# Performance work log

Measured on AMD Instinct MI355X. Metric: run time of the kernel, lower is better.

The kernel has to match this reference:

```python
import jax, jax.numpy as jnp
import numpy as np

B, N, D = 2, 1024, 1024
H, DH = 16, 64          # nhead, head_dim (D = H*DH)
FF = 4096               # dim_feedforward = 4*D
E = 8                   # num experts
EPS = 1e-5


def layer_norm(x, s, b):
    m = jnp.mean(x, -1, keepdims=True)
    v = jnp.mean((x - m) ** 2, -1, keepdims=True)
    return (x - m) * jax.lax.rsqrt(v + EPS) * s + b


def moe_gate(x, Wg):
    # top-1 gating: expert index + gate probability per token
    probs = jax.nn.softmax(x @ Wg, axis=-1)            # [B,N,E]
    idx = jnp.argmax(probs, axis=-1)                   # [B,N]
    gw = jnp.take_along_axis(probs, idx[..., None], -1)[..., 0]  # [B,N]
    return idx, gw


def moe_linear(x, W, b, idx, gw):
    # x:[B,N,Din], W:[E,Din,Dout], b:[E,Dout]; route each token to expert idx
    y = jnp.einsum('bnd,edh->bneh', x, W) + b          # [B,N,E,Dout]
    oh = jax.nn.one_hot(idx, E, dtype=x.dtype)         # [B,N,E]
    return jnp.einsum('bneh,bne->bnh', y, oh) * gw[..., None]


def setup_inputs() -> dict:
    key = jax.random.key(0)
    ks = jax.random.split(key, 8)
    g = lambda k, shape, sc: jax.random.normal(k, shape, jnp.float32) * sc
    inv_d = 1.0 / np.sqrt(D)
    return dict(
        src=g(ks[0], (B, N, D), 1.0),
        key_padding_mask=jnp.zeros((B, N), dtype=bool),
        Wg_attn=g(ks[1], (D, E), inv_d),
        Wqkv=g(ks[2], (E, D, 3 * D), inv_d), bqkv=jnp.zeros((E, 3 * D), jnp.float32),
        Wo=g(ks[3], (E, D, D), inv_d), bo=jnp.zeros((E, D), jnp.float32),
        Wg_ffn=g(ks[4], (D, E), inv_d),
        W1=g(ks[5], (E, D, FF), inv_d), b1=jnp.zeros((E, FF), jnp.float32),
        W2=g(ks[6], (E, FF, D), 1.0 / np.sqrt(FF)), b2=jnp.zeros((E, D), jnp.float32),
        ln1_s=jnp.ones((D,), jnp.float32), ln1_b=jnp.zeros((D,), jnp.float32),
        ln2_s=jnp.ones((D,), jnp.float32), ln2_b=jnp.zeros((D,), jnp.float32),
    )


def reference(src, key_padding_mask, Wg_attn, Wqkv, bqkv, Wo, bo,
              Wg_ffn, W1, b1, W2, b2, ln1_s, ln1_b, ln2_s, ln2_b):
    # attention mask: key_padding_mask.unsqueeze(1).unsqueeze(1) * -10000
    mask = jnp.where(key_padding_mask[:, None, None, :], -10000.0, 0.0).astype(src.dtype)

    # --- MoE self-attention (gate decided once, reused for qkv and dense) ---
    idx, gw = moe_gate(src, Wg_attn)
    qkv = moe_linear(src, Wqkv, bqkv, idx, gw)                 # [B,N,3D]
    q, k, v = jnp.split(qkv, 3, axis=-1)
    heads = lambda t: t.reshape(B, N, H, DH).transpose(0, 2, 1, 3)  # [B,H,N,DH]
    q, k, v = heads(q), heads(k), heads(v)
    scores = jnp.einsum('bhqd,bhkd->bhqk', q, k) / np.sqrt(DH) + mask
    probs = jax.nn.softmax(scores, axis=-1)
    ctx = jnp.einsum('bhqk,bhkd->bhqd', probs, v)
    ctx = ctx.transpose(0, 2, 1, 3).reshape(B, N, D)
    attn_out = moe_linear(ctx, Wo, bo, idx, gw)

    # post-norm residual
    x = layer_norm(src + attn_out, ln1_s, ln1_b)

    # --- MoE FFN (its own gate, shared across both linears) ---
    fidx, fgw = moe_gate(x, Wg_ffn)
    h = jax.nn.gelu(moe_linear(x, W1, b1, fidx, fgw))
    ffn = moe_linear(h, W2, b2, fidx, fgw)

    return layer_norm(x + ffn, ln2_s, ln2_b)
```

## Files before the change

### kernel.cpp

```cpp
#include <hip/hip_runtime.h>


#define B_   2
#define N_   1024
#define D_   1024
#define H_   16
#define DH_  64
#define FF_  4096
#define E_   8
#define NTOK 2048

typedef __attribute__((ext_vector_type(8))) short short8;
typedef __attribute__((ext_vector_type(8))) unsigned short ushort8;
typedef __attribute__((ext_vector_type(4))) unsigned short ushort4v;
typedef __attribute__((ext_vector_type(4))) float f32x4;

__device__ inline unsigned short f2bf(float f) {
  unsigned u = __float_as_uint(f);
  u += 0x7FFFu + ((u >> 16) & 1u);
  return (unsigned short)(u >> 16);
}

__device__ inline float gelu_tanh(float x) {
  float x3 = x * x * x;
  float t = tanhf(0.7978845608028654f * (x + 0.044715f * x3));
  return 0.5f * x * (1.0f + t);
}

__global__ __launch_bounds__(256) void gate_kernel(
    const float* __restrict__ X, const float* __restrict__ Wg,
    int* __restrict__ idx, float* __restrict__ gwv, int* __restrict__ cnt) {
  int t = blockIdx.x * 4 + (threadIdx.x >> 6);
  int lane = threadIdx.x & 63;
  const float* x = X + (size_t)t * D_;
  float acc[E_];
#pragma unroll
  for (int j = 0; j < E_; j++) acc[j] = 0.f;
#pragma unroll
  for (int i = 0; i < 16; i++) {
    int d = i * 64 + lane;
    float xv = x[d];
    const float4* w = (const float4*)(Wg + (size_t)d * E_);
    float4 w0 = w[0], w1 = w[1];
    acc[0] += xv * w0.x; acc[1] += xv * w0.y; acc[2] += xv * w0.z; acc[3] += xv * w0.w;
    acc[4] += xv * w1.x; acc[5] += xv * w1.y; acc[6] += xv * w1.z; acc[7] += xv * w1.w;
  }
#pragma unroll
  for (int o = 1; o < 64; o <<= 1) {
#pragma unroll
    for (int j = 0; j < E_; j++) acc[j] += __shfl_xor(acc[j], o, 64);
  }
  float m = acc[0]; int bi = 0;
#pragma unroll
  for (int j = 1; j < E_; j++) { if (acc[j] > m) { m = acc[j]; bi = j; } }
  float den = 0.f;
#pragma unroll
  for (int j = 0; j < E_; j++) den += expf(acc[j] - m);
  float gw = expf(acc[bi] - m) / den;
  if (lane == 0) { idx[t] = bi; gwv[t] = gw; atomicAdd(&cnt[bi], 1); }
}

__global__ __launch_bounds__(256) void route_kernel(
    const int* __restrict__ idx, const int* __restrict__ cnt,
    int* __restrict__ off, int* __restrict__ perm, int ntok) {
  __shared__ int loff[E_ + 1];
  __shared__ int lfill[E_];
  if (threadIdx.x == 0) {
    int s = 0;
    for (int e = 0; e < E_; e++) { loff[e] = s; s += cnt[e]; }
    loff[E_] = s;
  }
  if (threadIdx.x < E_) lfill[threadIdx.x] = 0;
  __syncthreads();
  for (int t = (int)threadIdx.x; t < ntok; t += 256) {
    int e = idx[t];
    int p = atomicAdd(&lfill[e], 1);
    perm[loff[e] + p] = t;
  }
  if (threadIdx.x < E_ + 1) off[threadIdx.x] = loff[threadIdx.x];
}

__global__ __launch_bounds__(256) void transpose_w_kernel(
    const float* __restrict__ W, unsigned short* __restrict__ WT, int K, int N) {
  __shared__ float T[64][68];
  int e = blockIdx.z;
  int n0 = blockIdx.x * 64, k0 = blockIdx.y * 64;
  int tid = threadIdx.x;
  {
    int kr = tid >> 4;
    int nc = (tid & 15) * 4;
#pragma unroll
    for (int j = 0; j < 4; j++) {
      int k = kr + j * 16;
      float4 v = *(const float4*)(W + ((size_t)e * K + k0 + k) * N + n0 + nc);
      *(float4*)&T[k][nc] = v;
    }
  }
  __syncthreads();
  {
    int n = tid & 63;
    int ko = (tid >> 6) * 16;
    ushort8 o0, o1;
#pragma unroll
    for (int i = 0; i < 8; i++) o0[i] = f2bf(T[ko + i][n]);
#pragma unroll
    for (int i = 0; i < 8; i++) o1[i] = f2bf(T[ko + 8 + i][n]);
    unsigned short* p = WT + ((size_t)e * N + n0 + n) * K + k0 + ko;
    *(ushort8*)p = o0;
    *(ushort8*)(p + 8) = o1;
  }
}

template <typename AT, int KS>
__global__ __launch_bounds__(256) void gemm_kernel(
    const AT* __restrict__ A, int ldA,
    const unsigned short* __restrict__ WT,
    const int* __restrict__ perm, const int* __restrict__ off,
    float* __restrict__ part, int K, int N) {
  __shared__ __align__(16) unsigned short As[128][40];
  __shared__ __align__(16) unsigned short Bs[128][40];
  __shared__ int toks[128];

  int e = blockIdx.y;
  int base = off[e];
  int cnt = off[e + 1] - base;
  int mt = blockIdx.z / KS;
  int kc = blockIdx.z % KS;
  int m0 = mt * 128;
  if (m0 >= cnt) return;
  int rows_valid = min(128, cnt - m0);
  int tid = threadIdx.x;
  if (tid < 128) {
    int r = (tid < rows_valid) ? tid : (rows_valid - 1);
    toks[tid] = perm[base + m0 + r];
  }
  int nb = blockIdx.x * 128;
  int lane = tid & 63, wave = tid >> 6;
  int wm = (wave >> 1) * 64, wn = (wave & 1) * 64;
  int lr = lane & 15, lg = lane >> 4;
  f32x4 acc[4][4];
#pragma unroll
  for (int m = 0; m < 4; m++)
#pragma unroll
    for (int n = 0; n < 4; n++) acc[m][n] = (f32x4){0.f, 0.f, 0.f, 0.f};
  int srow = tid >> 1, koff = (tid & 1) * 16;
  int KL = K / KS;
  int kbeg = kc * KL;
  __syncthreads();

  for (int k0 = kbeg; k0 < kbeg + KL; k0 += 32) {
    {
      const AT* ar = A + (size_t)toks[srow] * ldA + k0 + koff;
      ushort8 o0, o1;
      if constexpr (sizeof(AT) == 4) {
        const float* fa = (const float*)ar;
        float4 v0 = *(const float4*)(fa);
        float4 v1 = *(const float4*)(fa + 4);
        float4 v2 = *(const float4*)(fa + 8);
        float4 v3 = *(const float4*)(fa + 12);
        o0[0] = f2bf(v0.x); o0[1] = f2bf(v0.y); o0[2] = f2bf(v0.z); o0[3] = f2bf(v0.w);
        o0[4] = f2bf(v1.x); o0[5] = f2bf(v1.y); o0[6] = f2bf(v1.z); o0[7] = f2bf(v1.w);
        o1[0] = f2bf(v2.x); o1[1] = f2bf(v2.y); o1[2] = f2bf(v2.z); o1[3] = f2bf(v2.w);
        o1[4] = f2bf(v3.x); o1[5] = f2bf(v3.y); o1[6] = f2bf(v3.z); o1[7] = f2bf(v3.w);
      } else {
        o0 = *(const ushort8*)ar;
        o1 = *(const ushort8*)(ar + 8);
      }
      *(ushort8*)&As[srow][koff] = o0;
      *(ushort8*)&As[srow][koff + 8] = o1;
      const unsigned short* br = WT + ((size_t)e * N + nb + srow) * K + k0 + koff;
      *(ushort8*)&Bs[srow][koff] = *(const ushort8*)br;
      *(ushort8*)&Bs[srow][koff + 8] = *(const ushort8*)(br + 8);
    }
    __syncthreads();
    short8 av[4], bv[4];
#pragma unroll
    for (int m = 0; m < 4; m++) av[m] = *(const short8*)&As[wm + m * 16 + lr][lg * 8];
#pragma unroll
    for (int n = 0; n < 4; n++) bv[n] = *(const short8*)&Bs[wn + n * 16 + lr][lg * 8];
#pragma unroll
    for (int m = 0; m < 4; m++)
#pragma unroll
      for (int n = 0; n < 4; n++)
        acc[m][n] = __builtin_amdgcn_mfma_f32_16x16x32_bf16(av[m], bv[n], acc[m][n], 0, 0, 0);
    __syncthreads();
  }

  float* pr = part + (size_t)kc * ((size_t)NTOK * N);
#pragma unroll
  for (int n = 0; n < 4; n++) {
    int col = nb + wn + n * 16 + lr;
#pragma unroll
    for (int m = 0; m < 4; m++) {
#pragma unroll
      for (int reg = 0; reg < 4; reg++) {
        int r = wm + m * 16 + lg * 4 + reg;
        if (r < rows_valid)
          pr[(size_t)toks[r] * N + col] = acc[m][n][reg];
      }
    }
  }
}

template <int KS, bool GELU, bool OBF16>
__global__ __launch_bounds__(256) void reduce_kernel(
    const float* __restrict__ part, const float* __restrict__ bias,
    const float* __restrict__ gwv, const int* __restrict__ idx,
    void* __restrict__ out, int N) {
  int t = blockIdx.y;
  int n = (blockIdx.x * 256 + threadIdx.x) * 4;
  int e = idx[t];
  float gw = gwv[t];
  const float* p = part + (size_t)t * N + n;
  float4 a = *(const float4*)p;
#pragma unroll
  for (int k = 1; k < KS; k++) {
    float4 q = *(const float4*)(p + (size_t)k * NTOK * N);
    a.x += q.x; a.y += q.y; a.z += q.z; a.w += q.w;
  }
  float4 bv = *(const float4*)(bias + (size_t)e * N + n);
  a.x = (a.x + bv.x) * gw; a.y = (a.y + bv.y) * gw;
  a.z = (a.z + bv.z) * gw; a.w = (a.w + bv.w) * gw;
  if constexpr (GELU) {
    a.x = gelu_tanh(a.x); a.y = gelu_tanh(a.y);
    a.z = gelu_tanh(a.z); a.w = gelu_tanh(a.w);
  }
  if constexpr (OBF16) {
    ushort4v o;
    o[0] = f2bf(a.x); o[1] = f2bf(a.y); o[2] = f2bf(a.z); o[3] = f2bf(a.w);
    *(ushort4v*)((unsigned short*)out + (size_t)t * N + n) = o;
  } else {
    *(float4*)((float*)out + (size_t)t * N + n) = a;
  }
}

__global__ __launch_bounds__(256) void vtrans_kernel(
    const unsigned short* __restrict__ qkv, unsigned short* __restrict__ vT) {
  __shared__ __align__(16) unsigned short T[64][72];
  int bh = blockIdx.x;
  int b = bh >> 4, h = bh & 15;
  int tile = blockIdx.y;
  int tid = threadIdx.x;
  {
    int tk = tid >> 2, dof = (tid & 3) * 16;
    const unsigned short* p =
        qkv + ((size_t)(b * N_ + tile * 64 + tk)) * 3072 + 2048 + h * 64 + dof;
    *(ushort8*)&T[tk][dof] = *(const ushort8*)p;
    *(ushort8*)&T[tk][dof + 8] = *(const ushort8*)(p + 8);
  }
  __syncthreads();
  {
    int dh = tid >> 2, tof = (tid & 3) * 16;
    ushort8 o0, o1;
#pragma unroll
    for (int i = 0; i < 8; i++) o0[i] = T[tof + i][dh];
#pragma unroll
    for (int i = 0; i < 8; i++) o1[i] = T[tof + 8 + i][dh];
    unsigned short* q = vT + ((size_t)bh * 64 + dh) * N_ + tile * 64 + tof;
    *(ushort8*)q = o0;
    *(ushort8*)(q + 8) = o1;
  }
}

__global__ __launch_bounds__(256) void attn_kernel(
    const unsigned short* __restrict__ qkv, const unsigned short* __restrict__ vT,
    const unsigned char* __restrict__ kpm, unsigned short* __restrict__ ctx) {
  __shared__ __align__(16) unsigned short Qs[64][72];
  __shared__ __align__(16) unsigned short Ks[64][72];
  __shared__ __align__(16) unsigned short Vs[64][72];
  __shared__ __align__(16) unsigned short Ps[4][16][72];
  __shared__ float maskf[64];
  int qt = blockIdx.x, bh = blockIdx.y;
  int b = bh >> 4, h = bh & 15;
  int tid = threadIdx.x, lane = tid & 63, wave = tid >> 6;
  int lr = lane & 15, lg = lane >> 4;
  {
    int r = tid >> 2, dof = (tid & 3) * 16;
    const unsigned short* p = qkv + ((size_t)(b * N_ + qt * 64 + r)) * 3072 + h * 64 + dof;
    *(ushort8*)&Qs[r][dof] = *(const ushort8*)p;
    *(ushort8*)&Qs[r][dof + 8] = *(const ushort8*)(p + 8);
  }
  __syncthreads();
  short8 aq[2];
  aq[0] = *(const short8*)&Qs[wave * 16 + lr][lg * 8];
  aq[1] = *(const short8*)&Qs[wave * 16 + lr][32 + lg * 8];
  f32x4 O[4];
  float mrun[4], lrun[4];
#pragma unroll
  for (int r = 0; r < 4; r++) { mrun[r] = -1e30f; lrun[r] = 0.f; O[r] = (f32x4){0.f, 0.f, 0.f, 0.f}; }

  for (int kt = 0; kt < 16; kt++) {
    __syncthreads();
    {
      int r = tid >> 2, dof = (tid & 3) * 16;
      const unsigned short* p =
          qkv + ((size_t)(b * N_ + kt * 64 + r)) * 3072 + 1024 + h * 64 + dof;
      *(ushort8*)&Ks[r][dof] = *(const ushort8*)p;
      *(ushort8*)&Ks[r][dof + 8] = *(const ushort8*)(p + 8);
      const unsigned short* pv = vT + ((size_t)bh * 64 + r) * N_ + kt * 64 + dof;
      *(ushort8*)&Vs[r][dof] = *(const ushort8*)pv;
      *(ushort8*)&Vs[r][dof + 8] = *(const ushort8*)(pv + 8);
      if (tid < 64) maskf[tid] = kpm[b * N_ + kt * 64 + tid] ? -10000.f : 0.f;
    }
    __syncthreads();
    f32x4 S[4];
#pragma unroll
    for (int n = 0; n < 4; n++) {
      f32x4 s = (f32x4){0.f, 0.f, 0.f, 0.f};
#pragma unroll
      for (int ks = 0; ks < 2; ks++) {
        short8 bk = *(const short8*)&Ks[n * 16 + lr][ks * 32 + lg * 8];
        s = __builtin_amdgcn_mfma_f32_16x16x32_bf16(aq[ks], bk, s, 0, 0, 0);
      }
      float mv = maskf[n * 16 + lr];
#pragma unroll
      for (int r = 0; r < 4; r++) s[r] = s[r] * 0.125f + mv;
      S[n] = s;
    }
    float cur[4];
#pragma unroll
    for (int r = 0; r < 4; r++)
      cur[r] = fmaxf(fmaxf(S[0][r], S[1][r]), fmaxf(S[2][r], S[3][r]));
#pragma unroll
    for (int o = 1; o < 16; o <<= 1) {
#pragma unroll
      for (int r = 0; r < 4; r++) cur[r] = fmaxf(cur[r], __shfl_xor(cur[r], o, 64));
    }
    float alpha[4], rsum[4];
#pragma unroll
    for (int r = 0; r < 4; r++) {
      float mn = fmaxf(mrun[r], cur[r]);
      alpha[r] = expf(mrun[r] - mn);
      mrun[r] = mn;
      rsum[r] = 0.f;
    }
#pragma unroll
    for (int n = 0; n < 4; n++) {
#pragma unroll
      for (int r = 0; r < 4; r++) {
        S[n][r] = expf(S[n][r] - mrun[r]);
        rsum[r] += S[n][r];
      }
    }
#pragma unroll
    for (int o = 1; o < 16; o <<= 1) {
#pragma unroll
      for (int r = 0; r < 4; r++) rsum[r] += __shfl_xor(rsum[r], o, 64);
    }
#pragma unroll
    for (int r = 0; r < 4; r++) lrun[r] = lrun[r] * alpha[r] + rsum[r];
#pragma unroll
    for (int d = 0; d < 4; d++)
#pragma unroll
      for (int r = 0; r < 4; r++) O[d][r] *= alpha[r];
#pragma unroll
    for (int n = 0; n < 4; n++)
#pragma unroll
      for (int r = 0; r < 4; r++) Ps[wave][lg * 4 + r][n * 16 + lr] = f2bf(S[n][r]);
    short8 pf[2];
    pf[0] = *(const short8*)&Ps[wave][lr][lg * 8];
    pf[1] = *(const short8*)&Ps[wave][lr][32 + lg * 8];
#pragma unroll
    for (int d = 0; d < 4; d++) {
#pragma unroll
      for (int ks = 0; ks < 2; ks++) {
        short8 bv = *(const short8*)&Vs[d * 16 + lr][ks * 32 + lg * 8];
        O[d] = __builtin_amdgcn_mfma_f32_16x16x32_bf16(pf[ks], bv, O[d], 0, 0, 0);
      }
    }
  }
#pragma unroll
  for (int r = 0; r < 4; r++) lrun[r] = 1.f / lrun[r];
#pragma unroll
  for (int d = 0; d < 4; d++) {
#pragma unroll
    for (int r = 0; r < 4; r++) {
      int q = qt * 64 + wave * 16 + lg * 4 + r;
      int dh = d * 16 + lr;
      ctx[((size_t)(b * N_ + q)) * D_ + h * DH_ + dh] = f2bf(O[d][r] * lrun[r]);
    }
  }
}

template <int KS>
__global__ __launch_bounds__(256) void ln_reduce_kernel(
    const float* __restrict__ res, const float* __restrict__ part,
    const float* __restrict__ bias, const float* __restrict__ gwv,
    const int* __restrict__ idx,
    const float* __restrict__ S, const float* __restrict__ Bi,
    float* __restrict__ O) {
  int t = blockIdx.x, tid = threadIdx.x;
  int e = idx[t];
  float gw = gwv[t];
  const float* p = part + (size_t)t * D_ + tid * 4;
  float4 a = *(const float4*)p;
#pragma unroll
  for (int k = 1; k < KS; k++) {
    float4 q = *(const float4*)(p + (size_t)k * NTOK * D_);
    a.x += q.x; a.y += q.y; a.z += q.z; a.w += q.w;
  }
  float4 bv4 = *(const float4*)(bias + (size_t)e * D_ + tid * 4);
  float4 vr = ((const float4*)(res + (size_t)t * D_))[tid];
  float4 v;
  v.x = vr.x + (a.x + bv4.x) * gw;
  v.y = vr.y + (a.y + bv4.y) * gw;
  v.z = vr.z + (a.z + bv4.z) * gw;
  v.w = vr.w + (a.w + bv4.w) * gw;
  float s = v.x + v.y + v.z + v.w;
  float sq = v.x * v.x + v.y * v.y + v.z * v.z + v.w * v.w;
#pragma unroll
  for (int o = 1; o < 64; o <<= 1) {
    s += __shfl_xor(s, o, 64);
    sq += __shfl_xor(sq, o, 64);
  }
  __shared__ float ss[4], ssq[4];
  int wave = tid >> 6, lane = tid & 63;
  if (lane == 0) { ss[wave] = s; ssq[wave] = sq; }
  __syncthreads();
  float ts = ss[0] + ss[1] + ss[2] + ss[3];
  float tsq = ssq[0] + ssq[1] + ssq[2] + ssq[3];
  float mean = ts * (1.f / D_);
  float var = tsq * (1.f / D_) - mean * mean;
  float rs = rsqrtf(var + 1e-5f);
  float4 sv = ((const float4*)S)[tid];
  float4 bi = ((const float4*)Bi)[tid];
  float4 o;
  o.x = (v.x - mean) * rs * sv.x + bi.x;
  o.y = (v.y - mean) * rs * sv.y + bi.y;
  o.z = (v.z - mean) * rs * sv.z + bi.z;
  o.w = (v.w - mean) * rs * sv.w + bi.w;
  ((float4*)(O + (size_t)t * D_))[tid] = o;
}

extern "C" void kernel_launch(void* const* d_in, const int* in_sizes, int n_in,
                              void* d_out, int out_size, void* d_ws, size_t ws_size,
                              hipStream_t stream) {
  (void)in_sizes; (void)n_in; (void)out_size; (void)ws_size;
  const float* src     = (const float*)d_in[0];
  const unsigned char* kpm = (const unsigned char*)d_in[1];
  const float* Wg_attn = (const float*)d_in[2];
  const float* Wqkv    = (const float*)d_in[3];
  const float* bqkv    = (const float*)d_in[4];
  const float* Wo      = (const float*)d_in[5];
  const float* bo      = (const float*)d_in[6];
  const float* Wg_ffn  = (const float*)d_in[7];
  const float* W1      = (const float*)d_in[8];
  const float* b1      = (const float*)d_in[9];
  const float* W2      = (const float*)d_in[10];
  const float* b2      = (const float*)d_in[11];
  const float* ln1_s   = (const float*)d_in[12];
  const float* ln1_b   = (const float*)d_in[13];
  const float* ln2_s   = (const float*)d_in[14];
  const float* ln2_b   = (const float*)d_in[15];
  float* out = (float*)d_out;

  char* ws = (char*)d_ws;
  size_t o = 0;
  auto alloc = [&](size_t bytes) -> void* {
    void* p = ws + o;
    o += (bytes + 255) & ~(size_t)255;
    return p;
  };
  int* meta = (int*)alloc(256);
  int* cnt1 = meta;
  int* off1 = meta + 8;
  int* cnt2 = meta + 17;
  int* off2 = meta + 25;
  int* idx1 = (int*)alloc(NTOK * 4);
  float* gw1 = (float*)alloc(NTOK * 4);
  int* perm1 = (int*)alloc(NTOK * 4);
  int* idx2 = (int*)alloc(NTOK * 4);
  float* gw2 = (float*)alloc(NTOK * 4);
  int* perm2 = (int*)alloc(NTOK * 4);
  unsigned short* WT = (unsigned short*)alloc((size_t)E_ * FF_ * D_ * 2);
  unsigned short* qkvb = (unsigned short*)alloc((size_t)NTOK * 3072 * 2);
  unsigned short* vT = (unsigned short*)alloc((size_t)32 * 64 * N_ * 2);
  unsigned short* hbuf = qkvb;
  unsigned short* ctx = (unsigned short*)alloc((size_t)NTOK * D_ * 2);
  float* x = (float*)alloc((size_t)NTOK * D_ * 4);
  float* part = (float*)alloc((size_t)2 * NTOK * FF_ * 4);

  hipMemsetAsync(meta, 0, 256, stream);

  gate_kernel<<<512, 256, 0, stream>>>(src, Wg_attn, idx1, gw1, cnt1);
  route_kernel<<<1, 256, 0, stream>>>(idx1, cnt1, off1, perm1, NTOK);
  transpose_w_kernel<<<dim3(3072 / 64, 1024 / 64, 8), 256, 0, stream>>>(Wqkv, WT, 1024, 3072);
  gemm_kernel<float, 2><<<dim3(3072 / 128, 8, 32), 256, 0, stream>>>(
      src, 1024, WT, perm1, off1, part, 1024, 3072);
  reduce_kernel<2, false, true><<<dim3(3, NTOK), 256, 0, stream>>>(
      part, bqkv, gw1, idx1, qkvb, 3072);
  vtrans_kernel<<<dim3(32, 16), 256, 0, stream>>>(qkvb, vT);
  attn_kernel<<<dim3(16, 32), 256, 0, stream>>>(qkvb, vT, kpm, ctx);
  transpose_w_kernel<<<dim3(1024 / 64, 1024 / 64, 8), 256, 0, stream>>>(Wo, WT, 1024, 1024);
  gemm_kernel<unsigned short, 4><<<dim3(1024 / 128, 8, 64), 256, 0, stream>>>(
      ctx, 1024, WT, perm1, off1, part, 1024, 1024);
  ln_reduce_kernel<4><<<NTOK, 256, 0, stream>>>(
      src, part, bo, gw1, idx1, ln1_s, ln1_b, x);

  gate_kernel<<<512, 256, 0, stream>>>(x, Wg_ffn, idx2, gw2, cnt2);
  route_kernel<<<1, 256, 0, stream>>>(idx2, cnt2, off2, perm2, NTOK);
  transpose_w_kernel<<<dim3(4096 / 64, 1024 / 64, 8), 256, 0, stream>>>(W1, WT, 1024, 4096);
  gemm_kernel<float, 2><<<dim3(4096 / 128, 8, 32), 256, 0, stream>>>(
      x, 1024, WT, perm2, off2, part, 1024, 4096);
  reduce_kernel<2, true, true><<<dim3(4, NTOK), 256, 0, stream>>>(
      part, b1, gw2, idx2, hbuf, 4096);
  transpose_w_kernel<<<dim3(1024 / 64, 4096 / 64, 8), 256, 0, stream>>>(W2, WT, 4096, 1024);
  gemm_kernel<unsigned short, 4><<<dim3(1024 / 128, 8, 64), 256, 0, stream>>>(
      hbuf, 4096, WT, perm2, off2, part, 4096, 1024);
  ln_reduce_kernel<4><<<NTOK, 256, 0, stream>>>(
      x, part, b2, gw2, idx2, ln2_s, ln2_b, out);
}
```

Baseline: 748.2 us.

## Fuse weight transpose/bf16 conversion into grouped GEMM and enlarge M tile

Drops the separate transpose_w kernels that converted each expert weight to transposed bf16 in a workspace. The GEMM now reads fp32 weights directly, converts them to bf16 and writes them into an XOR-swizzled shared-memory tile. The block grows to 512 threads with a 256-row M tile, and the grid's z dimension is halved to match. This removes a full read and write pass over roughly 0.3 GB of expert weights, but each GEMM block now re-reads fp32 weights, and only tokens routed to used experts benefit.

```diff
diff --git a/kernel.cpp b/kernel.cpp
--- a/kernel.cpp
+++ b/kernel.cpp
@@ -80,63 +80,32 @@
   if (threadIdx.x < E_ + 1) off[threadIdx.x] = loff[threadIdx.x];
 }
 
-__global__ __launch_bounds__(256) void transpose_w_kernel(
-    const float* __restrict__ W, unsigned short* __restrict__ WT, int K, int N) {
-  __shared__ float T[64][68];
-  int e = blockIdx.z;
-  int n0 = blockIdx.x * 64, k0 = blockIdx.y * 64;
-  int tid = threadIdx.x;
-  {
-    int kr = tid >> 4;
-    int nc = (tid & 15) * 4;
-#pragma unroll
-    for (int j = 0; j < 4; j++) {
-      int k = kr + j * 16;
-      float4 v = *(const float4*)(W + ((size_t)e * K + k0 + k) * N + n0 + nc);
-      *(float4*)&T[k][nc] = v;
-    }
-  }
-  __syncthreads();
-  {
-    int n = tid & 63;
-    int ko = (tid >> 6) * 16;
-    ushort8 o0, o1;
-#pragma unroll
-    for (int i = 0; i < 8; i++) o0[i] = f2bf(T[ko + i][n]);
-#pragma unroll
-    for (int i = 0; i < 8; i++) o1[i] = f2bf(T[ko + 8 + i][n]);
-    unsigned short* p = WT + ((size_t)e * N + n0 + n) * K + k0 + ko;
-    *(ushort8*)p = o0;
-    *(ushort8*)(p + 8) = o1;
-  }
-}
-
 template <typename AT, int KS>
-__global__ __launch_bounds__(256) void gemm_kernel(
+__global__ __launch_bounds__(512, 2) void gemm_kernel(
     const AT* __restrict__ A, int ldA,
-    const unsigned short* __restrict__ WT,
+    const float* __restrict__ W,
     const int* __restrict__ perm, const int* __restrict__ off,
     float* __restrict__ part, int K, int N) {
-  __shared__ __align__(16) unsigned short As[128][40];
+  __shared__ __align__(16) unsigned short As[256][40];
   __shared__ __align__(16) unsigned short Bs[128][40];
-  __shared__ int toks[128];
+  __shared__ int toks[256];
 
   int e = blockIdx.y;
   int base = off[e];
   int cnt = off[e + 1] - base;
   int mt = blockIdx.z / KS;
   int kc = blockIdx.z % KS;
-  int m0 = mt * 128;
+  int m0 = mt * 256;
   if (m0 >= cnt) return;
-  int rows_valid = min(128, cnt - m0);
+  int rows_valid = min(256, cnt - m0);
   int tid = threadIdx.x;
-  if (tid < 128) {
+  if (tid < 256) {
     int r = (tid < rows_valid) ? tid : (rows_valid - 1);
     toks[tid] = perm[base + m0 + r];
   }
   int nb = blockIdx.x * 128;
   int lane = tid & 63, wave = tid >> 6;
-  int wm = (wave >> 1) * 64, wn = (wave & 1) * 64;
+  int wm = (wave & 3) * 64, wn = (wave >> 2) * 64;
   int lr = lane & 15, lg = lane >> 4;
   f32x4 acc[4][4];
 #pragma unroll
@@ -144,6 +113,8 @@
 #pragma unroll
     for (int n = 0; n < 4; n++) acc[m][n] = (f32x4){0.f, 0.f, 0.f, 0.f};
   int srow = tid >> 1, koff = (tid & 1) * 16;
+  int k2 = (tid & 15) * 2, cB = tid >> 4;
+  int n0 = cB * 4;
   int KL = K / KS;
   int kbeg = kc * KL;
   __syncthreads();
@@ -168,16 +139,31 @@
       }
       *(ushort8*)&As[srow][koff] = o0;
       *(ushort8*)&As[srow][koff + 8] = o1;
-      const unsigned short* br = WT + ((size_t)e * N + nb + srow) * K + k0 + koff;
-      *(ushort8*)&Bs[srow][koff] = *(const ushort8*)br;
-      *(ushort8*)&Bs[srow][koff + 8] = *(const ushort8*)(br + 8);
+    }
+    {
+      const float* w0 = W + ((size_t)e * K + k0 + k2) * N + nb + n0;
+      float4 r0 = *(const float4*)w0;
+      float4 r1 = *(const float4*)(w0 + N);
+      float lo[4] = {r0.x, r0.y, r0.z, r0.w};
+      float hi[4] = {r1.x, r1.y, r1.z, r1.w};
+#pragma unroll
+      for (int j = 0; j < 4; j++) {
+        int n = n0 + j;
+        int sc = (((k2 >> 3) ^ ((n >> 2) & 3)) << 3) | (k2 & 7);
+        unsigned v = (unsigned)f2bf(lo[j]) | ((unsigned)f2bf(hi[j]) << 16);
+        *(unsigned*)&Bs[n][sc] = v;
+      }
     }
     __syncthreads();
     short8 av[4], bv[4];
 #pragma unroll
     for (int m = 0; m < 4; m++) av[m] = *(const short8*)&As[wm + m * 16 + lr][lg * 8];
 #pragma unroll
-    for (int n = 0; n < 4; n++) bv[n] = *(const short8*)&Bs[wn + n * 16 + lr][lg * 8];
+    for (int n = 0; n < 4; n++) {
+      int nn = wn + n * 16 + lr;
+      int blk = lg ^ ((nn >> 2) & 3);
+      bv[n] = *(const short8*)&Bs[nn][blk * 8];
+    }
 #pragma unroll
     for (int m = 0; m < 4; m++)
 #pragma unroll
@@ -472,7 +458,6 @@
   int* idx2 = (int*)alloc(NTOK * 4);
   float* gw2 = (float*)alloc(NTOK * 4);
   int* perm2 = (int*)alloc(NTOK * 4);
-  unsigned short* WT = (unsigned short*)alloc((size_t)E_ * FF_ * D_ * 2);
   unsigned short* qkvb = (unsigned short*)alloc((size_t)NTOK * 3072 * 2);
   unsigned short* vT = (unsigned short*)alloc((size_t)32 * 64 * N_ * 2);
   unsigned short* hbuf = qkvb;
@@ -484,29 +469,25 @@
 
   gate_kernel<<<512, 256, 0, stream>>>(src, Wg_attn, idx1, gw1, cnt1);
   route_kernel<<<1, 256, 0, stream>>>(idx1, cnt1, off1, perm1, NTOK);
-  transpose_w_kernel<<<dim3(3072 / 64, 1024 / 64, 8), 256, 0, stream>>>(Wqkv, WT, 1024, 3072);
-  gemm_kernel<float, 2><<<dim3(3072 / 128, 8, 32), 256, 0, stream>>>(
-      src, 1024, WT, perm1, off1, part, 1024, 3072);
+  gemm_kernel<float, 2><<<dim3(3072 / 128, 8, 16), 512, 0, stream>>>(
+      src, 1024, Wqkv, perm1, off1, part, 1024, 3072);
   reduce_kernel<2, false, true><<<dim3(3, NTOK), 256, 0, stream>>>(
       part, bqkv, gw1, idx1, qkvb, 3072);
   vtrans_kernel<<<dim3(32, 16), 256, 0, stream>>>(qkvb, vT);
   attn_kernel<<<dim3(16, 32), 256, 0, stream>>>(qkvb, vT, kpm, ctx);
-  transpose_w_kernel<<<dim3(1024 / 64, 1024 / 64, 8), 256, 0, stream>>>(Wo, WT, 1024, 1024);
-  gemm_kernel<unsigned short, 4><<<dim3(1024 / 128, 8, 64), 256, 0, stream>>>(
-      ctx, 1024, WT, perm1, off1, part, 1024, 1024);
+  gemm_kernel<unsigned short, 4><<<dim3(1024 / 128, 8, 32), 512, 0, stream>>>(
+      ctx, 1024, Wo, perm1, off1, part, 1024, 1024);
   ln_reduce_kernel<4><<<NTOK, 256, 0, stream>>>(
       src, part, bo, gw1, idx1, ln1_s, ln1_b, x);
 
   gate_kernel<<<512, 256, 0, stream>>>(x, Wg_ffn, idx2, gw2, cnt2);
   route_kernel<<<1, 256, 0, stream>>>(idx2, cnt2, off2, perm2, NTOK);
-  transpose_w_kernel<<<dim3(4096 / 64, 1024 / 64, 8), 256, 0, stream>>>(W1, WT, 1024, 4096);
-  gemm_kernel<float, 2><<<dim3(4096 / 128, 8, 32), 256, 0, stream>>>(
-      x, 1024, WT, perm2, off2, part, 1024, 4096);
+  gemm_kernel<float, 2><<<dim3(4096 / 128, 8, 16), 512, 0, stream>>>(
+      x, 1024, W1, perm2, off2, part, 1024, 4096);
   reduce_kernel<2, true, true><<<dim3(4, NTOK), 256, 0, stream>>>(
       part, b1, gw2, idx2, hbuf, 4096);
-  transpose_w_kernel<<<dim3(1024 / 64, 4096 / 64, 8), 256, 0, stream>>>(W2, WT, 4096, 1024);
-  gemm_kernel<unsigned short, 4><<<dim3(1024 / 128, 8, 64), 256, 0, stream>>>(
-      hbuf, 4096, WT, perm2, off2, part, 4096, 1024);
+  gemm_kernel<unsigned short, 4><<<dim3(1024 / 128, 8, 32), 512, 0, stream>>>(
+      hbuf, 4096, W2, perm2, off2, part, 4096, 1024);
   ln_reduce_kernel<4><<<NTOK, 256, 0, stream>>>(
       x, part, b2, gw2, idx2, ln2_s, ln2_b, out);
 }
```

Result: faster. 698.9 us (-6.6%).
